# Performance work log

Measured on AMD Instinct MI355X. Metric: run time of the kernel, lower is better.

## Reference

```python
import jax, jax.numpy as jnp
import numpy as np

N = 50000
E = 800000
FEAT = 128
COND = 64
HID = 128
LAT = 64


def setup_inputs() -> dict:
    key = jax.random.key(0)
    ks = jax.random.split(key, 16)
    inp = {
        "feature": jax.random.normal(ks[0], (N, FEAT), jnp.float32),
        "condition": jax.random.normal(ks[1], (N, COND), jnp.float32),
        "edge_index": jax.random.randint(ks[2], (2, E), 0, N, jnp.int64 if jax.config.jax_enable_x64 else jnp.int32),
        "noise": jax.random.normal(ks[3], (N, LAT), jnp.float32),
        # GCNConv params (glorot-style scale)
        "W_f2h": jax.random.normal(ks[4], (FEAT, HID), jnp.float32) * (1.0 / np.sqrt(FEAT)),
        "b_f2h": jnp.zeros((HID,), jnp.float32),
        "W_c2h": jax.random.normal(ks[5], (COND, HID), jnp.float32) * (1.0 / np.sqrt(COND)),
        "b_c2h": jnp.zeros((HID,), jnp.float32),
        "W_h2h": jax.random.normal(ks[6], (2 * HID, HID), jnp.float32) * (1.0 / np.sqrt(2 * HID)),
        "b_h2h": jnp.zeros((HID,), jnp.float32),
        "W_mean": jax.random.normal(ks[7], (HID, LAT), jnp.float32) * (1.0 / np.sqrt(HID)),
        "b_mean": jnp.zeros((LAT,), jnp.float32),
        "W_logvar": jax.random.normal(ks[8], (HID, LAT), jnp.float32) * (1.0 / np.sqrt(HID)),
        "b_logvar": jnp.zeros((LAT,), jnp.float32),
    }
    return inp


def _gcn_norm(edge_index, n):
    # add self-loops, compute symmetric normalization deg^-1/2 * deg^-1/2
    loop = jnp.arange(n, dtype=edge_index.dtype)
    src = jnp.concatenate([edge_index[0], loop])
    dst = jnp.concatenate([edge_index[1], loop])
    deg = jax.ops.segment_sum(jnp.ones_like(src, jnp.float32), dst, num_segments=n)
    dinv = jnp.where(deg > 0, jax.lax.rsqrt(deg), 0.0)
    norm = dinv[src] * dinv[dst]  # [E+N]
    return src, dst, norm


def _gcn_conv(x, W, b, src, dst, norm, n):
    h = x @ W                                  # [N, out]
    msg = h[src] * norm[:, None]               # gather + scale, [E+N, out]
    out = jax.ops.segment_sum(msg, dst, num_segments=n)
    return out + b


def reference(feature, condition, edge_index, noise,
              W_f2h, b_f2h, W_c2h, b_c2h, W_h2h, b_h2h,
              W_mean, b_mean, W_logvar, b_logvar):
    n = feature.shape[0]
    src, dst, norm = _gcn_norm(edge_index, n)
    f2h = jnp.tanh(_gcn_conv(feature, W_f2h, b_f2h, src, dst, norm, n))
    c2h = jnp.tanh(_gcn_conv(condition, W_c2h, b_c2h, src, dst, norm, n))
    h = jnp.concatenate([f2h, c2h], axis=1)
    h = jnp.tanh(_gcn_conv(h, W_h2h, b_h2h, src, dst, norm, n))
    mean = _gcn_conv(h, W_mean, b_mean, src, dst, norm, n)
    logvar = _gcn_conv(h, W_logvar, b_logvar, src, dst, norm, n)
    z = noise * jnp.exp(0.5 * logvar) + mean
    return (z, mean, logvar)
```

## Files before the change

kernel.cpp:

```cpp
#include <hip/hip_runtime.h>
#include <math.h>

namespace {

constexpr int N = 50000;
constexpr int E = 800000;

typedef __attribute__((ext_vector_type(8))) short short8;
typedef __attribute__((ext_vector_type(4))) float f32x4;


__device__ inline unsigned short f2bf(float f) {
  unsigned int b = __float_as_uint(f);
  unsigned int r = (b + 0x7fffu + ((b >> 16) & 1u)) >> 16;
  return (unsigned short)r;
}
__device__ inline float bf_lo(unsigned int u) { return __uint_as_float(u << 16); }
__device__ inline float bf_hi(unsigned int u) { return __uint_as_float(u & 0xffff0000u); }
__device__ inline unsigned int pack2(float a, float b) {
  return (unsigned int)f2bf(a) | ((unsigned int)f2bf(b) << 16);
}


__global__ void zero_int(int* p, int n) {
  int i = blockIdx.x * blockDim.x + threadIdx.x;
  if (i < n) p[i] = 0;
}

__global__ void count_deg_rank(const int* __restrict__ dst, int* __restrict__ cnt,
                               int* __restrict__ rank, int e) {
  int i = blockIdx.x * blockDim.x + threadIdx.x;
  if (i < e) rank[i] = atomicAdd(&cnt[dst[i]], 1);
}

__global__ void block_sums(const int* __restrict__ cnt, int* __restrict__ bsum, int n) {
  int tid = threadIdx.x;
  int i = blockIdx.x * 256 + tid;
  int v = (i < n) ? cnt[i] : 0;
  for (int off = 32; off > 0; off >>= 1) v += __shfl_down(v, off, 64);
  __shared__ int sred[4];
  if ((tid & 63) == 0) sred[tid >> 6] = v;
  __syncthreads();
  if (tid == 0) bsum[blockIdx.x] = sred[0] + sred[1] + sred[2] + sred[3];
}

__global__ void scan_bsums(int* bsum, int nb) {
  if (threadIdx.x == 0 && blockIdx.x == 0) {
    int run = 0;
    for (int b = 0; b < nb; ++b) { int t = bsum[b]; bsum[b] = run; run += t; }
  }
}

__global__ void scan_chunks(const int* __restrict__ cnt, const int* __restrict__ bsum,
                            int* __restrict__ row_ptr, int n) {
  __shared__ int s[256];
  int tid = threadIdx.x;
  int i = blockIdx.x * 256 + tid;
  int v = (i < n) ? cnt[i] : 0;
  s[tid] = v;
  __syncthreads();
  for (int d = 1; d < 256; d <<= 1) {
    int t = (tid >= d) ? s[tid - d] : 0;
    __syncthreads();
    s[tid] += t;
    __syncthreads();
  }
  if (i < n) {
    int excl = bsum[blockIdx.x] + s[tid] - v;
    row_ptr[i] = excl;
    if (i == n - 1) row_ptr[n] = excl + v;
  }
}

__global__ void compute_dinv(const int* __restrict__ cnt, float* __restrict__ dinv, int n) {
  int i = blockIdx.x * blockDim.x + threadIdx.x;
  if (i < n) dinv[i] = rsqrtf((float)(cnt[i] + 1));
}

__global__ __launch_bounds__(256) void scatter_xcd(const int* __restrict__ src,
                                                   const int* __restrict__ dst,
                                                   const int* __restrict__ rank,
                                                   const int* __restrict__ row_ptr,
                                                   int* __restrict__ csr_src) {
  constexpr int RANGE = (N + 7) / 8;
  int r = blockIdx.x & 7;
  int lo = r * RANGE;
  int hi = lo + RANGE;
  int nb = gridDim.x >> 3;
  int bi = blockIdx.x >> 3;
  for (int e = bi * 256 + threadIdx.x; e < E; e += nb * 256) {
    int d = dst[e];
    if (d >= lo && d < hi) {
      csr_src[row_ptr[d] + rank[e]] = src[e];
    }
  }
}


__global__ void cvt_cond(const float* __restrict__ in, unsigned short* __restrict__ out, int n) {
  int t = blockIdx.x * blockDim.x + threadIdx.x;
  if (t >= n * 8) return;
  int i = t >> 3, j = t & 7;
  const float* s = in + (size_t)i * 64 + j * 8;
  float4 a = *(const float4*)s;
  float4 b = *(const float4*)(s + 4);
  uint4 o;
  o.x = pack2(a.x, a.y);
  o.y = pack2(a.z, a.w);
  o.z = pack2(b.x, b.y);
  o.w = pack2(b.z, b.w);
  *(uint4*)(out + (size_t)i * 192 + 128 + j * 8) = o;
}

__global__ void pack_w(const float* __restrict__ W1, int s1,
                       const float* __restrict__ W2, int s2, int split,
                       int ksteps, unsigned short* __restrict__ out) {
  int t = blockIdx.x * blockDim.x + threadIdx.x;
  int total = ksteps * 8 * 64;
  if (t >= total) return;
  int ks = t >> 9;
  int ct = (t >> 6) & 7;
  int l = t & 63;
  int k0 = ks * 32 + ((l >> 4) << 3);
  int col = ct * 16 + (l & 15);
  const float* src;
  int c;
  if (col < split) { src = W1 + col; c = s1; }
  else { src = W2 + (col - split); c = s2; }
  unsigned short* o = out + (size_t)t * 8;
#pragma unroll
  for (int i = 0; i < 8; ++i) o[i] = f2bf(src[(size_t)(k0 + i) * c]);
}

__global__ void make_bcat(const float* __restrict__ bm, const float* __restrict__ bl,
                          float* __restrict__ bcat) {
  int j = threadIdx.x;
  if (j < 64) bcat[j] = bm[j];
  else if (j < 128) bcat[j] = bl[j - 64];
}


template <int K, int EPI, bool F32A>
__global__ __launch_bounds__(256) void gemm_mfma(const void* __restrict__ Av, int lda,
                                                 const unsigned short* __restrict__ Wp,
                                                 const float* __restrict__ bias,
                                                 unsigned short* __restrict__ C, int ldc, int n) {
  constexpr int KSTEPS = K / 32;
  int tid = threadIdx.x;
  int w = tid >> 6;
  int l = tid & 63;
  int r0 = blockIdx.x * 128 + w * 32;
  int arow = l & 15;
  int kgrp = l >> 4;

  f32x4 acc[2][8];
#pragma unroll
  for (int m = 0; m < 2; ++m)
#pragma unroll
    for (int ct = 0; ct < 8; ++ct) acc[m][ct] = (f32x4)(0.f);

  int ra0 = min(r0 + arow, n - 1);
  int ra1 = min(r0 + 16 + arow, n - 1);

#pragma unroll 1
  for (int ks = 0; ks < KSTEPS; ++ks) {
    short8 a0, a1;
    if (F32A) {
      const float* p0 = (const float*)Av + (size_t)ra0 * lda + kgrp * 8 + ks * 32;
      const float* p1 = (const float*)Av + (size_t)ra1 * lda + kgrp * 8 + ks * 32;
      float4 x0 = *(const float4*)p0, y0 = *(const float4*)(p0 + 4);
      float4 x1 = *(const float4*)p1, y1 = *(const float4*)(p1 + 4);
      unsigned int u[4];
      u[0] = pack2(x0.x, x0.y); u[1] = pack2(x0.z, x0.w);
      u[2] = pack2(y0.x, y0.y); u[3] = pack2(y0.z, y0.w);
      a0 = *(const short8*)u;
      u[0] = pack2(x1.x, x1.y); u[1] = pack2(x1.z, x1.w);
      u[2] = pack2(y1.x, y1.y); u[3] = pack2(y1.z, y1.w);
      a1 = *(const short8*)u;
    } else {
      a0 = *(const short8*)((const unsigned short*)Av + (size_t)ra0 * lda + kgrp * 8 + ks * 32);
      a1 = *(const short8*)((const unsigned short*)Av + (size_t)ra1 * lda + kgrp * 8 + ks * 32);
    }
    const short8* pb = (const short8*)Wp + (size_t)(ks * 8) * 64 + l;
#pragma unroll
    for (int ct = 0; ct < 8; ++ct) {
      short8 b = pb[ct * 64];
      acc[0][ct] = __builtin_amdgcn_mfma_f32_16x16x32_bf16(a0, b, acc[0][ct], 0, 0, 0);
      acc[1][ct] = __builtin_amdgcn_mfma_f32_16x16x32_bf16(a1, b, acc[1][ct], 0, 0, 0);
    }
  }

  int ccol = l & 15;
  int crow = (l >> 4) * 4;
#pragma unroll
  for (int ct = 0; ct < 8; ++ct) {
    int col = ct * 16 + ccol;
    float bv = (EPI == 1) ? bias[col] : 0.f;
#pragma unroll
    for (int m = 0; m < 2; ++m) {
#pragma unroll
      for (int r = 0; r < 4; ++r) {
        int row = r0 + m * 16 + crow + r;
        if (row < n) {
          float v = acc[m][ct][r];
          if (EPI == 1) v = tanhf(v + bv);
          C[(size_t)row * ldc + col] = f2bf(v);
        }
      }
    }
  }
}


#define ACC8_INIT(ACC, U, D)                                        \
  ACC[0] = D * bf_lo(U.x); ACC[1] = D * bf_hi(U.x);                 \
  ACC[2] = D * bf_lo(U.y); ACC[3] = D * bf_hi(U.y);                 \
  ACC[4] = D * bf_lo(U.z); ACC[5] = D * bf_hi(U.z);                 \
  ACC[6] = D * bf_lo(U.w); ACC[7] = D * bf_hi(U.w);

#define ACC8_FMA(ACC, U, D)                                         \
  ACC[0] = fmaf(D, bf_lo(U.x), ACC[0]); ACC[1] = fmaf(D, bf_hi(U.x), ACC[1]); \
  ACC[2] = fmaf(D, bf_lo(U.y), ACC[2]); ACC[3] = fmaf(D, bf_hi(U.y), ACC[3]); \
  ACC[4] = fmaf(D, bf_lo(U.z), ACC[4]); ACC[5] = fmaf(D, bf_hi(U.z), ACC[5]); \
  ACC[6] = fmaf(D, bf_lo(U.w), ACC[6]); ACC[7] = fmaf(D, bf_hi(U.w), ACC[7]);

#define EDGE_WALK(LANES)                                            \
  int e = e0;                                                       \
  for (; e + 2 <= e1; e += 2) {                                     \
    int s0 = csr_src[e], s1 = csr_src[e + 1];                       \
    float d0 = dinv[s0], d1 = dinv[s1];                             \
    uint4 u0 = X4[(size_t)s0 * LANES + lane];                       \
    uint4 u1 = X4[(size_t)s1 * LANES + lane];                       \
    ACC8_FMA(acc, u0, d0)                                           \
    ACC8_FMA(acc2, u1, d1)                                          \
  }                                                                 \
  if (e < e1) {                                                     \
    int s0 = csr_src[e];                                            \
    float d0 = dinv[s0];                                            \
    uint4 u0 = X4[(size_t)s0 * LANES + lane];                       \
    ACC8_FMA(acc, u0, d0)                                           \
  }                                                                 \
  _Pragma("unroll")                                                 \
  for (int j = 0; j < 8; ++j) acc[j] += acc2[j];


__global__ __launch_bounds__(192) void prop192(const unsigned short* __restrict__ X,
                                               unsigned short* __restrict__ f2h_out,
                                               unsigned short* __restrict__ pc_out,
                                               const int* __restrict__ row_ptr,
                                               const int* __restrict__ csr_src,
                                               const float* __restrict__ dinv,
                                               const float* __restrict__ b_f2h, int n) {
  constexpr int LANES = 24;
  int lane = threadIdx.x % LANES;
  int rloc = threadIdx.x / LANES;
  int i = blockIdx.x * 8 + rloc;
  if (i >= n) return;
  const uint4* X4 = (const uint4*)X;
  float di = dinv[i];
  float acc[8], acc2[8];
  {
    uint4 u = X4[(size_t)i * LANES + lane];
    ACC8_INIT(acc, u, di)
  }
#pragma unroll
  for (int j = 0; j < 8; ++j) acc2[j] = 0.f;
  int e0 = row_ptr[i], e1 = row_ptr[i + 1];
  EDGE_WALK(24)
  if (lane < 16) {
    float out[8];
#pragma unroll
    for (int j = 0; j < 8; ++j) out[j] = tanhf(fmaf(di, acc[j], b_f2h[lane * 8 + j]));
    uint4 o;
    o.x = pack2(out[0], out[1]); o.y = pack2(out[2], out[3]);
    o.z = pack2(out[4], out[5]); o.w = pack2(out[6], out[7]);
    *(uint4*)(f2h_out + (size_t)i * 256 + lane * 8) = o;
  } else {
    uint4 o;
    o.x = pack2(di * acc[0], di * acc[1]); o.y = pack2(di * acc[2], di * acc[3]);
    o.z = pack2(di * acc[4], di * acc[5]); o.w = pack2(di * acc[6], di * acc[7]);
    *(uint4*)(pc_out + (size_t)i * 64 + (lane - 16) * 8) = o;
  }
}


__global__ __launch_bounds__(256) void prop128(const unsigned short* __restrict__ X,
                                               unsigned short* __restrict__ Y,
                                               const int* __restrict__ row_ptr,
                                               const int* __restrict__ csr_src,
                                               const float* __restrict__ dinv,
                                               const float* __restrict__ bias, int n) {
  constexpr int LANES = 16;
  int lane = threadIdx.x % LANES;
  int rloc = threadIdx.x / LANES;
  int i = blockIdx.x * 16 + rloc;
  if (i >= n) return;
  const uint4* X4 = (const uint4*)X;
  float di = dinv[i];
  float acc[8], acc2[8];
  {
    uint4 u = X4[(size_t)i * LANES + lane];
    ACC8_INIT(acc, u, di)
  }
#pragma unroll
  for (int j = 0; j < 8; ++j) acc2[j] = 0.f;
  int e0 = row_ptr[i], e1 = row_ptr[i + 1];
  EDGE_WALK(16)
  float out[8];
#pragma unroll
  for (int j = 0; j < 8; ++j) out[j] = tanhf(fmaf(di, acc[j], bias[lane * 8 + j]));
  uint4 o;
  o.x = pack2(out[0], out[1]); o.y = pack2(out[2], out[3]);
  o.z = pack2(out[4], out[5]); o.w = pack2(out[6], out[7]);
  *(uint4*)(Y + (size_t)i * 128 + lane * 8) = o;
}


__global__ __launch_bounds__(256) void prop_fin_bf(const unsigned short* __restrict__ X,
                                                   const int* __restrict__ row_ptr,
                                                   const int* __restrict__ csr_src,
                                                   const float* __restrict__ dinv,
                                                   const float* __restrict__ bcat,
                                                   const float* __restrict__ noise,
                                                   float* __restrict__ out, int n) {
  constexpr int LANES = 16;
  int lane = threadIdx.x & 15;
  int rloc = threadIdx.x >> 4;
  int i = blockIdx.x * 16 + rloc;
  if (i >= n) return;
  const uint4* X4 = (const uint4*)X;
  float di = dinv[i];
  float acc[8], acc2[8];
  {
    uint4 u = X4[(size_t)i * LANES + lane];
    ACC8_INIT(acc, u, di)
  }
#pragma unroll
  for (int j = 0; j < 8; ++j) acc2[j] = 0.f;
  int e0 = row_ptr[i], e1 = row_ptr[i + 1];
  EDGE_WALK(16)
  float v[8];
#pragma unroll
  for (int j = 0; j < 8; ++j) v[j] = fmaf(di, acc[j], bcat[lane * 8 + j]);
  float p[8];
#pragma unroll
  for (int j = 0; j < 8; ++j) p[j] = __shfl_xor(v[j], 8);
  size_t n64 = (size_t)n * 64;
  if (lane < 8) {
    const float* nz = noise + (size_t)i * 64 + lane * 8;
    float z[8];
#pragma unroll
    for (int j = 0; j < 8; ++j) z[j] = fmaf(nz[j], expf(0.5f * p[j]), v[j]);
    float* zp = out + (size_t)i * 64 + lane * 8;
    *(float4*)zp = make_float4(z[0], z[1], z[2], z[3]);
    *(float4*)(zp + 4) = make_float4(z[4], z[5], z[6], z[7]);
    float* mp = out + n64 + (size_t)i * 64 + lane * 8;
    *(float4*)mp = make_float4(v[0], v[1], v[2], v[3]);
    *(float4*)(mp + 4) = make_float4(v[4], v[5], v[6], v[7]);
  } else {
    float* lp = out + 2 * n64 + (size_t)i * 64 + (lane - 8) * 8;
    *(float4*)lp = make_float4(v[0], v[1], v[2], v[3]);
    *(float4*)(lp + 4) = make_float4(v[4], v[5], v[6], v[7]);
  }
}

}

extern "C" void kernel_launch(void* const* d_in, const int* in_sizes, int n_in,
                              void* d_out, int out_size, void* d_ws, size_t ws_size,
                              hipStream_t stream) {
  const float* feature   = (const float*)d_in[0];
  const float* condition = (const float*)d_in[1];
  const int*   ei        = (const int*)d_in[2];
  const float* noise     = (const float*)d_in[3];
  const float* W_f2h     = (const float*)d_in[4];
  const float* b_f2h     = (const float*)d_in[5];
  const float* W_c2h     = (const float*)d_in[6];
  const float* b_c2h     = (const float*)d_in[7];
  const float* W_h2h     = (const float*)d_in[8];
  const float* b_h2h     = (const float*)d_in[9];
  const float* W_mean    = (const float*)d_in[10];
  const float* b_mean    = (const float*)d_in[11];
  const float* W_logvar  = (const float*)d_in[12];
  const float* b_logvar  = (const float*)d_in[13];

  const int* src = ei;
  const int* dst = ei + E;

  char* p = (char*)d_ws;
  auto alloc = [&](size_t bytes) {
    char* q = p;
    p += (bytes + 255) & ~(size_t)255;
    return q;
  };
  unsigned short* buf192 = (unsigned short*)alloc((size_t)N * 192 * 2);
  unsigned short* bufU   = (unsigned short*)alloc((size_t)N * 128 * 2);
  unsigned short* catbuf = (unsigned short*)alloc((size_t)N * 256 * 2);
  unsigned short* Pcbf   = (unsigned short*)alloc((size_t)N * 64 * 2);
  int*   cnt     = (int*)alloc((size_t)N * 4);
  int*   rank    = (int*)alloc((size_t)E * 4);
  int*   row_ptr = (int*)alloc((size_t)(N + 1) * 4);
  int*   csr_src = (int*)alloc((size_t)E * 4);
  int*   bsum    = (int*)alloc(256 * 4);
  float* dinv    = (float*)alloc((size_t)N * 4);
  unsigned short* Wf2h_p = (unsigned short*)alloc(4 * 512 * 8 * 2);
  unsigned short* Wc2h_p = (unsigned short*)alloc(2 * 512 * 8 * 2);
  unsigned short* Wh2h_p = (unsigned short*)alloc(8 * 512 * 8 * 2);
  unsigned short* Wcat_p = (unsigned short*)alloc(4 * 512 * 8 * 2);
  float* bcat    = (float*)alloc(128 * 4);
  unsigned short* hbuf = buf192;
  (void)ws_size; (void)in_sizes; (void)n_in; (void)out_size;

  int nb = (N + 255) / 256;

  zero_int<<<(N + 255) / 256, 256, 0, stream>>>(cnt, N);
  count_deg_rank<<<(E + 255) / 256, 256, 0, stream>>>(dst, cnt, rank, E);
  block_sums<<<nb, 256, 0, stream>>>(cnt, bsum, N);
  scan_bsums<<<1, 64, 0, stream>>>(bsum, nb);
  scan_chunks<<<nb, 256, 0, stream>>>(cnt, bsum, row_ptr, N);
  compute_dinv<<<(N + 255) / 256, 256, 0, stream>>>(cnt, dinv, N);
  scatter_xcd<<<1024, 256, 0, stream>>>(src, dst, rank, row_ptr, csr_src);

  cvt_cond<<<(N * 8 + 255) / 256, 256, 0, stream>>>(condition, buf192, N);
  pack_w<<<(4 * 512 + 255) / 256, 256, 0, stream>>>(W_f2h, 128, nullptr, 0, 128, 4, Wf2h_p);
  pack_w<<<(2 * 512 + 255) / 256, 256, 0, stream>>>(W_c2h, 128, nullptr, 0, 128, 2, Wc2h_p);
  pack_w<<<(8 * 512 + 255) / 256, 256, 0, stream>>>(W_h2h, 128, nullptr, 0, 128, 8, Wh2h_p);
  pack_w<<<(4 * 512 + 255) / 256, 256, 0, stream>>>(W_mean, 64, W_logvar, 64, 64, 4, Wcat_p);
  make_bcat<<<1, 128, 0, stream>>>(b_mean, b_logvar, bcat);

  int ggrid = (N + 127) / 128;

  gemm_mfma<128, 0, true><<<ggrid, 256, 0, stream>>>(feature, 128, Wf2h_p, nullptr, buf192, 192, N);
  prop192<<<(N + 7) / 8, 192, 0, stream>>>(buf192, catbuf, Pcbf, row_ptr, csr_src, dinv, b_f2h, N);
  gemm_mfma<64, 1, false><<<ggrid, 256, 0, stream>>>(Pcbf, 64, Wc2h_p, b_c2h, catbuf + 128, 256, N);
  gemm_mfma<256, 0, false><<<ggrid, 256, 0, stream>>>(catbuf, 256, Wh2h_p, nullptr, bufU, 128, N);
  prop128<<<(N + 15) / 16, 256, 0, stream>>>(bufU, hbuf, row_ptr, csr_src, dinv, b_h2h, N);
  gemm_mfma<128, 0, false><<<ggrid, 256, 0, stream>>>(hbuf, 128, Wcat_p, nullptr, bufU, 128, N);
  prop_fin_bf<<<(N + 15) / 16, 256, 0, stream>>>(bufU, row_ptr, csr_src, dinv, bcat, noise,
                                                 (float*)d_out, N);
}
```

Baseline: 298.7 us.

## Prescale GEMM outputs by source dinv and unroll edge gather four-wide

The source-side normalization factor dinv[src] is folded into the producers: the GEMM epilogues (new EPI==2 mode) and the condition conversion multiply each row by dinv. The propagation kernels then no longer gather dinv per edge and just sum bf16 rows. The edge walk is also unrolled to four independent accumulators to put more gathers in flight. This moves one rounding step earlier (scaling before the bf16 store) and raises register pressure in the propagation kernels.

New measurement: 318.8 us. +6.8%, slower.

```diff
diff --git a/kernel.cpp b/kernel.cpp
--- a/kernel.cpp
+++ b/kernel.cpp
@@ -97,18 +97,20 @@
 }
 
 
-__global__ void cvt_cond(const float* __restrict__ in, unsigned short* __restrict__ out, int n) {
+__global__ void cvt_cond(const float* __restrict__ in, const float* __restrict__ dinv,
+                         unsigned short* __restrict__ out, int n) {
   int t = blockIdx.x * blockDim.x + threadIdx.x;
   if (t >= n * 8) return;
   int i = t >> 3, j = t & 7;
+  float di = dinv[i];
   const float* s = in + (size_t)i * 64 + j * 8;
   float4 a = *(const float4*)s;
   float4 b = *(const float4*)(s + 4);
   uint4 o;
-  o.x = pack2(a.x, a.y);
-  o.y = pack2(a.z, a.w);
-  o.z = pack2(b.x, b.y);
-  o.w = pack2(b.z, b.w);
+  o.x = pack2(di * a.x, di * a.y);
+  o.y = pack2(di * a.z, di * a.w);
+  o.z = pack2(di * b.x, di * b.y);
+  o.w = pack2(di * b.z, di * b.w);
   *(uint4*)(out + (size_t)i * 192 + 128 + j * 8) = o;
 }
 
@@ -143,7 +145,7 @@
 template <int K, int EPI, bool F32A>
 __global__ __launch_bounds__(256) void gemm_mfma(const void* __restrict__ Av, int lda,
                                                  const unsigned short* __restrict__ Wp,
-                                                 const float* __restrict__ bias,
+                                                 const float* __restrict__ bias_or_scale,
                                                  unsigned short* __restrict__ C, int ldc, int n) {
   constexpr int KSTEPS = K / 32;
   int tid = threadIdx.x;
@@ -195,7 +197,7 @@
 #pragma unroll
   for (int ct = 0; ct < 8; ++ct) {
     int col = ct * 16 + ccol;
-    float bv = (EPI == 1) ? bias[col] : 0.f;
+    float bv = (EPI == 1) ? bias_or_scale[col] : 0.f;
 #pragma unroll
     for (int m = 0; m < 2; ++m) {
 #pragma unroll
@@ -204,6 +206,7 @@
         if (row < n) {
           float v = acc[m][ct][r];
           if (EPI == 1) v = tanhf(v + bv);
+          if (EPI == 2) v = v * bias_or_scale[row];
           C[(size_t)row * ldc + col] = f2bf(v);
         }
       }
@@ -212,36 +215,42 @@
 }
 
 
-#define ACC8_INIT(ACC, U, D)                                        \
-  ACC[0] = D * bf_lo(U.x); ACC[1] = D * bf_hi(U.x);                 \
-  ACC[2] = D * bf_lo(U.y); ACC[3] = D * bf_hi(U.y);                 \
-  ACC[4] = D * bf_lo(U.z); ACC[5] = D * bf_hi(U.z);                 \
-  ACC[6] = D * bf_lo(U.w); ACC[7] = D * bf_hi(U.w);
-
-#define ACC8_FMA(ACC, U, D)                                         \
-  ACC[0] = fmaf(D, bf_lo(U.x), ACC[0]); ACC[1] = fmaf(D, bf_hi(U.x), ACC[1]); \
-  ACC[2] = fmaf(D, bf_lo(U.y), ACC[2]); ACC[3] = fmaf(D, bf_hi(U.y), ACC[3]); \
-  ACC[4] = fmaf(D, bf_lo(U.z), ACC[4]); ACC[5] = fmaf(D, bf_hi(U.z), ACC[5]); \
-  ACC[6] = fmaf(D, bf_lo(U.w), ACC[6]); ACC[7] = fmaf(D, bf_hi(U.w), ACC[7]);
-
-#define EDGE_WALK(LANES)                                            \
-  int e = e0;                                                       \
-  for (; e + 2 <= e1; e += 2) {                                     \
-    int s0 = csr_src[e], s1 = csr_src[e + 1];                       \
-    float d0 = dinv[s0], d1 = dinv[s1];                             \
-    uint4 u0 = X4[(size_t)s0 * LANES + lane];                       \
-    uint4 u1 = X4[(size_t)s1 * LANES + lane];                       \
-    ACC8_FMA(acc, u0, d0)                                           \
-    ACC8_FMA(acc2, u1, d1)                                          \
-  }                                                                 \
-  if (e < e1) {                                                     \
-    int s0 = csr_src[e];                                            \
-    float d0 = dinv[s0];                                            \
-    uint4 u0 = X4[(size_t)s0 * LANES + lane];                       \
-    ACC8_FMA(acc, u0, d0)                                           \
-  }                                                                 \
-  _Pragma("unroll")                                                 \
-  for (int j = 0; j < 8; ++j) acc[j] += acc2[j];
+#define ACC8_SET(ACC, U)                                  \
+  ACC[0] = bf_lo(U.x); ACC[1] = bf_hi(U.x);               \
+  ACC[2] = bf_lo(U.y); ACC[3] = bf_hi(U.y);               \
+  ACC[4] = bf_lo(U.z); ACC[5] = bf_hi(U.z);               \
+  ACC[6] = bf_lo(U.w); ACC[7] = bf_hi(U.w);
+
+#define ACC8_ADD(ACC, U)                                  \
+  ACC[0] += bf_lo(U.x); ACC[1] += bf_hi(U.x);             \
+  ACC[2] += bf_lo(U.y); ACC[3] += bf_hi(U.y);             \
+  ACC[4] += bf_lo(U.z); ACC[5] += bf_hi(U.z);             \
+  ACC[6] += bf_lo(U.w); ACC[7] += bf_hi(U.w);
+
+#define EDGE_WALK(LANES)                                                \
+  float acc1[8], acc2[8], acc3[8];                                      \
+  _Pragma("unroll")                                                     \
+  for (int j = 0; j < 8; ++j) { acc1[j] = 0.f; acc2[j] = 0.f; acc3[j] = 0.f; } \
+  int e = e0;                                                           \
+  for (; e + 4 <= e1; e += 4) {                                         \
+    int s0 = csr_src[e], s1 = csr_src[e + 1];                           \
+    int s2 = csr_src[e + 2], s3 = csr_src[e + 3];                       \
+    uint4 u0 = X4[(size_t)s0 * LANES + lane];                           \
+    uint4 u1 = X4[(size_t)s1 * LANES + lane];                           \
+    uint4 u2 = X4[(size_t)s2 * LANES + lane];                           \
+    uint4 u3 = X4[(size_t)s3 * LANES + lane];                           \
+    ACC8_ADD(acc, u0)                                                   \
+    ACC8_ADD(acc1, u1)                                                  \
+    ACC8_ADD(acc2, u2)                                                  \
+    ACC8_ADD(acc3, u3)                                                  \
+  }                                                                     \
+  for (; e < e1; ++e) {                                                 \
+    int s0 = csr_src[e];                                                \
+    uint4 u0 = X4[(size_t)s0 * LANES + lane];                           \
+    ACC8_ADD(acc, u0)                                                   \
+  }                                                                     \
+  _Pragma("unroll")                                                     \
+  for (int j = 0; j < 8; ++j) acc[j] = (acc[j] + acc1[j]) + (acc2[j] + acc3[j]);
 
 
 __global__ __launch_bounds__(192) void prop192(const unsigned short* __restrict__ X,
@@ -258,13 +267,11 @@
   if (i >= n) return;
   const uint4* X4 = (const uint4*)X;
   float di = dinv[i];
-  float acc[8], acc2[8];
+  float acc[8];
   {
     uint4 u = X4[(size_t)i * LANES + lane];
-    ACC8_INIT(acc, u, di)
-  }
-#pragma unroll
-  for (int j = 0; j < 8; ++j) acc2[j] = 0.f;
+    ACC8_SET(acc, u)
+  }
   int e0 = row_ptr[i], e1 = row_ptr[i + 1];
   EDGE_WALK(24)
   if (lane < 16) {
@@ -297,13 +304,11 @@
   if (i >= n) return;
   const uint4* X4 = (const uint4*)X;
   float di = dinv[i];
-  float acc[8], acc2[8];
+  float acc[8];
   {
     uint4 u = X4[(size_t)i * LANES + lane];
-    ACC8_INIT(acc, u, di)
-  }
-#pragma unroll
-  for (int j = 0; j < 8; ++j) acc2[j] = 0.f;
+    ACC8_SET(acc, u)
+  }
   int e0 = row_ptr[i], e1 = row_ptr[i + 1];
   EDGE_WALK(16)
   float out[8];
@@ -330,13 +335,11 @@
   if (i >= n) return;
   const uint4* X4 = (const uint4*)X;
   float di = dinv[i];
-  float acc[8], acc2[8];
+  float acc[8];
   {
     uint4 u = X4[(size_t)i * LANES + lane];
-    ACC8_INIT(acc, u, di)
-  }
-#pragma unroll
-  for (int j = 0; j < 8; ++j) acc2[j] = 0.f;
+    ACC8_SET(acc, u)
+  }
   int e0 = row_ptr[i], e1 = row_ptr[i + 1];
   EDGE_WALK(16)
   float v[8];
@@ -421,7 +424,7 @@
   compute_dinv<<<(N + 255) / 256, 256, 0, stream>>>(cnt, dinv, N);
   scatter_xcd<<<1024, 256, 0, stream>>>(src, dst, rank, row_ptr, csr_src);
 
-  cvt_cond<<<(N * 8 + 255) / 256, 256, 0, stream>>>(condition, buf192, N);
+  cvt_cond<<<(N * 8 + 255) / 256, 256, 0, stream>>>(condition, dinv, buf192, N);
   pack_w<<<(4 * 512 + 255) / 256, 256, 0, stream>>>(W_f2h, 128, nullptr, 0, 128, 4, Wf2h_p);
   pack_w<<<(2 * 512 + 255) / 256, 256, 0, stream>>>(W_c2h, 128, nullptr, 0, 128, 2, Wc2h_p);
   pack_w<<<(8 * 512 + 255) / 256, 256, 0, stream>>>(W_h2h, 128, nullptr, 0, 128, 8, Wh2h_p);
@@ -430,12 +433,12 @@
 
   int ggrid = (N + 127) / 128;
 
-  gemm_mfma<128, 0, true><<<ggrid, 256, 0, stream>>>(feature, 128, Wf2h_p, nullptr, buf192, 192, N);
+  gemm_mfma<128, 2, true><<<ggrid, 256, 0, stream>>>(feature, 128, Wf2h_p, dinv, buf192, 192, N);
   prop192<<<(N + 7) / 8, 192, 0, stream>>>(buf192, catbuf, Pcbf, row_ptr, csr_src, dinv, b_f2h, N);
   gemm_mfma<64, 1, false><<<ggrid, 256, 0, stream>>>(Pcbf, 64, Wc2h_p, b_c2h, catbuf + 128, 256, N);
-  gemm_mfma<256, 0, false><<<ggrid, 256, 0, stream>>>(catbuf, 256, Wh2h_p, nullptr, bufU, 128, N);
+  gemm_mfma<256, 2, false><<<ggrid, 256, 0, stream>>>(catbuf, 256, Wh2h_p, dinv, bufU, 128, N);
   prop128<<<(N + 15) / 16, 256, 0, stream>>>(bufU, hbuf, row_ptr, csr_src, dinv, b_h2h, N);
-  gemm_mfma<128, 0, false><<<ggrid, 256, 0, stream>>>(hbuf, 128, Wcat_p, nullptr, bufU, 128, N);
+  gemm_mfma<128, 2, false><<<ggrid, 256, 0, stream>>>(hbuf, 128, Wcat_p, dinv, bufU, 128, N);
   prop_fin_bf<<<(N + 15) / 16, 256, 0, stream>>>(bufU, row_ptr, csr_src, dinv, bcat, noise,
                                                  (float*)d_out, N);
 }
```
